# Performance work log

Measured on AMD Instinct MI355X. Metric: run time of the kernel, lower is better.

## Reference

```python
import jax, jax.numpy as jnp
import numpy as np

NODE_W, EDGE_W, HEADS = 512, 32, 8
DOT = NODE_W // HEADS
CLIP_MIN, CLIP_MAX = -5.0, 5.0
B, N = 4, 1024


def setup_inputs() -> dict:
    key = jax.random.key(0)
    ks = jax.random.split(key, 12)
    s = 0.02
    return {
        "nodes": jax.random.normal(ks[0], (B, N, NODE_W), dtype=jnp.float32),
        "edges": jax.random.normal(ks[1], (B, N, N, EDGE_W), dtype=jnp.float32),
        "Wq": jax.random.normal(ks[2], (NODE_W, NODE_W), dtype=jnp.float32) * s,
        "bq": jnp.zeros((NODE_W,), dtype=jnp.float32),
        "Wk": jax.random.normal(ks[3], (NODE_W, NODE_W), dtype=jnp.float32) * s,
        "bk": jnp.zeros((NODE_W,), dtype=jnp.float32),
        "Wv": jax.random.normal(ks[4], (NODE_W, NODE_W), dtype=jnp.float32) * s,
        "bv": jnp.zeros((NODE_W,), dtype=jnp.float32),
        "Wg": jax.random.normal(ks[5], (EDGE_W, HEADS), dtype=jnp.float32) * s,
        "bg": jnp.zeros((HEADS,), dtype=jnp.float32),
        "We": jax.random.normal(ks[6], (EDGE_W, HEADS), dtype=jnp.float32) * s,
        "be": jnp.zeros((HEADS,), dtype=jnp.float32),
    }


def reference(nodes, edges, Wq, bq, Wk, bk, Wv, bv, Wg, bg, We, be):
    b, n, _ = nodes.shape
    # projections, reshaped to [B, N, dot_dim, heads] as in the torch .view
    q = (nodes @ Wq + bq).reshape(b, n, DOT, HEADS)
    k = (nodes @ Wk + bk).reshape(b, n, DOT, HEADS)
    v = (nodes @ Wv + bv).reshape(b, n, DOT, HEADS)
    # raw scores [B, L, M, heads], scaled and clipped
    H = jnp.einsum('bldh,bmdh->blmh', q, k) / (DOT ** 0.5)
    H = jnp.clip(H, CLIP_MIN, CLIP_MAX)
    # edge bias and gate, each [B, N, N, heads]
    e = edges @ We + be
    g = edges @ Wg + bg
    H = H + e
    # softmax over key axis (dim=2), sigmoid gate multiply
    A = jax.nn.sigmoid(g) * jax.nn.softmax(H, axis=2)
    # dropout is identity in eval/deterministic mode
    attn = jnp.einsum('blmh,bmdh->bldh', A, v).reshape(b, n, NODE_W)
    return attn, H
```

## Files before the change

kernel.cpp:

```cpp
#include <hip/hip_runtime.h>
#include <hip/hip_bf16.h>
#include <stdint.h>

typedef float  f32x4  __attribute__((ext_vector_type(4)));
typedef float  f32x2  __attribute__((ext_vector_type(2)));
typedef short  bf16x8 __attribute__((ext_vector_type(8)));
typedef short  bf16x4 __attribute__((ext_vector_type(4)));

#define MFMA16(A,B,C) __builtin_amdgcn_mfma_f32_16x16x32_bf16(A,B,C,0,0,0)

__device__ __forceinline__ short f2bf(float x){
    union { float f; uint32_t u; } v; v.f = x;
    uint32_t r = v.u + 0x7fffu + ((v.u >> 16) & 1u);
    return (short)(r >> 16);
}
__device__ __forceinline__ float bf2f(short x){
    union { uint32_t u; float f; } v; v.u = ((uint32_t)(uint16_t)x) << 16;
    return v.f;
}
__device__ __forceinline__ uint32_t cvt2(float lo, float hi){
    __hip_bfloat162 t = __float22bfloat162_rn(float2{lo, hi});
    union { __hip_bfloat162 b; uint32_t u; } c; c.b = t; return c.u;
}
__device__ __forceinline__ bf16x8 pack8(f32x4 a, f32x4 b){
    union { uint32_t u[4]; bf16x8 s; } c;
    c.u[0] = cvt2(a[0], a[1]); c.u[1] = cvt2(a[2], a[3]);
    c.u[2] = cvt2(b[0], b[1]); c.u[3] = cvt2(b[2], b[3]);
    return c.s;
}

__global__ void k_prep_wt(const float* __restrict__ Wq, const float* __restrict__ Wk,
                          const float* __restrict__ Wv, short* __restrict__ WT){
    int blk = blockIdx.x;
    int w  = blk >> 6;
    int t  = blk & 63;
    int k0 = (t >> 3) << 6;
    int o0 = (t & 7) << 6;
    const float* W = (w == 0) ? Wq : ((w == 1) ? Wk : Wv);
    __shared__ float tile[64][65];
    int tx = threadIdx.x & 63, ty = threadIdx.x >> 6;
    #pragma unroll
    for (int i = 0; i < 64; i += 4)
        tile[ty + i][tx] = W[(size_t)(k0 + ty + i) * 512 + o0 + tx];
    __syncthreads();
    short* out = WT + (size_t)w * 512 * 512;
    #pragma unroll
    for (int i = 0; i < 64; i += 4)
        out[(size_t)(o0 + ty + i) * 512 + k0 + tx] = f2bf(tile[tx][ty + i]);
}

__global__ void k_prep_wcat(const float* __restrict__ We, const float* __restrict__ Wg,
                            const float* __restrict__ be, const float* __restrict__ bg,
                            short* __restrict__ WcatT, float* __restrict__ bcat){
    int t = threadIdx.x;
    int ch = t >> 5, c = t & 31;
    float v = (ch < 8) ? We[c * 8 + ch] : Wg[c * 8 + (ch - 8)];
    WcatT[ch * 32 + c] = f2bf(v);
    if (t < 16) bcat[t] = (t < 8) ? be[t] : bg[t - 8];
}

__global__ void k_prep_nodes(const float* __restrict__ nodes, short* __restrict__ nb){
    size_t i = ((size_t)blockIdx.x * 256 + threadIdx.x) * 8;
    f32x4 a = *(const f32x4*)(nodes + i);
    f32x4 b = *(const f32x4*)(nodes + i + 4);
    *(bf16x8*)(nb + i) = pack8(a, b);
}

__global__ void k_qkv(const short* __restrict__ nodesbf, const short* __restrict__ WT,
                      const float* __restrict__ bq, const float* __restrict__ bk,
                      const float* __restrict__ bv,
                      short* __restrict__ qb, short* __restrict__ kb, short* __restrict__ vTb){
    int bx = blockIdx.x;
    int lt = bx & 255;
    int ob = bx >> 8;
    int wave = threadIdx.x >> 6, lane = threadIdx.x & 63;
    int lr = lane & 15, lg = lane >> 4;
    int row0 = lt << 4;
    int og = ob * 256 + wave * 64;
    int w  = og >> 9;
    int oo = og & 511;
    int dhalf = ob & 1;

    const short* Wp = WT + (size_t)w * 512 * 512;
    f32x4 acc[4] = {};
    const short* arow = nodesbf + (size_t)(row0 + lr) * 512 + lg * 8;
    #pragma unroll
    for (int kk = 0; kk < 16; ++kk){
        bf16x8 af = *(const bf16x8*)(arow + kk * 32);
        #pragma unroll
        for (int s = 0; s < 4; ++s){
            const short* bp = Wp + (size_t)(oo + s * 16 + lr) * 512 + kk * 32 + lg * 8;
            bf16x8 bfv = *(const bf16x8*)bp;
            acc[s] = MFMA16(af, bfv, acc[s]);
        }
    }
    const float* bias = (w == 0) ? bq : ((w == 1) ? bk : bv);
    int b  = row0 >> 10;
    int lbase = row0 & 1023;

    __shared__ short St[4096];
    #pragma unroll
    for (int s = 0; s < 4; ++s){
        int o = oo + s * 16 + lr;
        float bsv = bias[o];
        int h = o & 7, dd = (o >> 3) & 31;
        #pragma unroll
        for (int r = 0; r < 4; ++r){
            short sv = f2bf(acc[s][r] + bsv);
            int l = lg * 4 + r;
            if (w < 2) St[(l << 8) + (h << 5) + dd] = sv;
            else       St[(h << 9) + (dd << 4) + l] = sv;
        }
    }
    __syncthreads();
    int t = threadIdx.x;
    bf16x8 v0 = *(const bf16x8*)&St[t * 16];
    bf16x8 v1 = *(const bf16x8*)&St[t * 16 + 8];
    if (w < 2){
        short* dst = (w == 0) ? qb : kb;
        int l = t >> 4, h = (t >> 1) & 7, dd0 = (t & 1) << 4;
        size_t a = ((size_t)(b * 8 + h) * 1024 + lbase + l) * 64 + dhalf * 32 + dd0;
        *(bf16x8*)(dst + a)     = v0;
        *(bf16x8*)(dst + a + 8) = v1;
    } else {
        int h = t >> 5, dd = t & 31;
        size_t a = ((size_t)(b * 8 + h) * 64 + dhalf * 32 + dd) * 1024 + lbase;
        *(bf16x8*)(vTb + a)     = v0;
        *(bf16x8*)(vTb + a + 8) = v1;
    }
}

__global__ __launch_bounds__(256, 3) void k_hsg(
        const float* __restrict__ edges, const short* __restrict__ qb,
        const short* __restrict__ kb, const short* __restrict__ WcatT,
        const float* __restrict__ bcat,
        float* __restrict__ Hout, short* __restrict__ Pb,
        float* __restrict__ psum){
    int bx = blockIdx.x;
    int j  = bx & 7;  int b = j >> 1;
    int rest = bx >> 3;
    int mt = rest & 15;
    int lt = (rest >> 4) | ((j & 1) << 5);
    int w = threadIdx.x >> 6, lane = threadIdx.x & 63;
    int lr = lane & 15, lg = lane >> 4;
    int l0 = lt << 4;
    int mg = (mt << 6) + (w << 4);
    const size_t bl0 = (size_t)(b * 1024 + l0);

    __shared__ short eg[4][4096];
    char* egw = (char*)&eg[w][0];
    const int swz = (lr & 7) << 4;

    f32x4 ebA[4][2], ebB[4][2];
    #pragma unroll
    for (int i = 0; i < 4; ++i){
        const float* ep = edges + ((bl0 + i) * 1024 + mg + lr) * 32 + lg * 8;
        ebA[i][0] = *(const f32x4*)ep;
        ebA[i][1] = *(const f32x4*)(ep + 4);
    }

    f32x4 S[8] = {};
    #pragma unroll
    for (int h = 0; h < 8; ++h){
        #pragma unroll
        for (int half = 0; half < 2; ++half){
            bf16x8 kf = *(const bf16x8*)(kb + ((size_t)(b * 8 + h) * 1024 + mg + lr) * 64 + half * 32 + lg * 8);
            bf16x8 qf = *(const bf16x8*)(qb + ((size_t)(b * 8 + h) * 1024 + l0 + lr) * 64 + half * 32 + lg * 8);
            S[h] = MFMA16(kf, qf, S[h]);
        }
    }

    bf16x8 wf = *(const bf16x8*)(WcatT + lr * 32 + lg * 8);
    f32x4  bc = *(const f32x4*)(bcat + lg * 4);
    f32x4 zero = {0.f, 0.f, 0.f, 0.f};
    #pragma unroll
    for (int c = 0; c < 4; ++c){
        if (c < 3){
            #pragma unroll
            for (int i = 0; i < 4; ++i){
                const float* ep = edges + ((bl0 + (c + 1) * 4 + i) * 1024 + mg + lr) * 32 + lg * 8;
                if (c & 1){ ebA[i][0] = *(const f32x4*)ep; ebA[i][1] = *(const f32x4*)(ep + 4); }
                else      { ebB[i][0] = *(const f32x4*)ep; ebB[i][1] = *(const f32x4*)(ep + 4); }
            }
        }
        #pragma unroll
        for (int i = 0; i < 4; ++i){
            int l = c * 4 + i;
            f32x4 e0 = (c & 1) ? ebB[i][0] : ebA[i][0];
            f32x4 e1 = (c & 1) ? ebB[i][1] : ebA[i][1];
            f32x4 d = MFMA16(wf, pack8(e0, e1), zero);
            union { uint32_t u[2]; bf16x4 v; } dv;
            dv.u[0] = cvt2(d[0] + bc[0], d[1] + bc[1]);
            dv.u[1] = cvt2(d[2] + bc[2], d[3] + bc[3]);
            int bw = (l * 512 + lr * 32 + lg * 8) ^ ((l & 7) << 4);
            *(bf16x4*)(egw + bw) = dv.v;
        }
    }

    float exu[4][8], pgv[4][8];
    #pragma unroll
    for (int rr = 0; rr < 4; ++rr){
        int base = lr * 512 + (4 * lg + rr) * 32;
        bf16x8 e8 = *(const bf16x8*)(egw + ((base)      ^ swz));
        bf16x8 g8 = *(const bf16x8*)(egw + ((base + 16) ^ swz));
        float Hv[8];
        #pragma unroll
        for (int h = 0; h < 8; ++h){
            float s = S[h][rr] * 0.125f;
            s = fminf(fmaxf(s, -5.f), 5.f);
            float hv = s + bf2f(e8[h]);
            Hv[h] = hv;
            float ex = __expf(hv);
            exu[rr][h] = ex;
            float sg = __builtin_amdgcn_rcpf(1.f + __expf(-bf2f(g8[h])));
            pgv[rr][h] = ex * sg;
        }
        float* hp = Hout + (bl0 + lr) * 8192 + (size_t)(mg + 4 * lg + rr) * 8;
        f32x4 h0 = {Hv[0], Hv[1], Hv[2], Hv[3]};
        f32x4 h1 = {Hv[4], Hv[5], Hv[6], Hv[7]};
        *(f32x4*)hp       = h0;
        *(f32x4*)(hp + 4) = h1;
    }

    size_t ptile = ((size_t)(b * 8) * 64 + lt) * 64 + (mt * 4 + w);
    size_t psbase = (((size_t)(b * 64 + lt) * 16 + mt) * 4 + w) * 128;
    #pragma unroll
    for (int h = 0; h < 8; ++h){
        union { uint32_t u[2]; bf16x4 v; } pv;
        pv.u[0] = cvt2(pgv[0][h], pgv[1][h]);
        pv.u[1] = cvt2(pgv[2][h], pgv[3][h]);
        *(bf16x4*)(Pb + (ptile + (size_t)h * 4096) * 256 + lr * 16 + lg * 4) = pv.v;
        float t = exu[0][h] + exu[1][h] + exu[2][h] + exu[3][h];
        t += __shfl_xor(t, 16);
        t += __shfl_xor(t, 32);
        if (lg == 0) psum[psbase + h * 16 + lr] = t;
    }
}

__global__ void k_pv(const short* __restrict__ Pb, const float* __restrict__ psum,
                     const short* __restrict__ vTb, float* __restrict__ attn){
    int bx = blockIdx.x;
    int j  = bx & 7;  int b = j >> 1;
    int lt = ((j & 1) << 5) | (bx >> 3);
    int h    = threadIdx.x >> 6;
    int lane = threadIdx.x & 63;
    int lr = lane & 15, lg = lane >> 4;
    int l0 = lt << 4;

    const short* Pbase = Pb  + (((size_t)(b * 8 + h) * 64 + lt) * 64) * 256;
    const short* vbase = vTb + (size_t)(b * 8 + h) * 65536;

    f32x4 O[4] = {};
    for (int ks = 0; ks < 32; ++ks){
        bf16x8 pf = *(const bf16x8*)(Pbase + (ks * 2 + (lg >> 1)) * 256 + lr * 16 + (lg & 1) * 8);
        #pragma unroll
        for (int dt = 0; dt < 4; ++dt){
            bf16x8 vf = *(const bf16x8*)(vbase + (size_t)(dt * 16 + lr) * 1024 + ks * 32 + lg * 8);
            O[dt] = MFMA16(vf, pf, O[dt]);
        }
    }

    const float* pp = psum + ((size_t)(b * 64 + lt) * 16) * 512;
    float ds = 0.f;
    #pragma unroll
    for (int c = 0; c < 16; ++c)
        ds += pp[(c * 4 + lg) * 128 + h * 16 + lr];
    ds += __shfl_xor(ds, 16);
    ds += __shfl_xor(ds, 32);
    float inv = __builtin_amdgcn_rcpf(ds);

    __shared__ float Os[16][516];
    #pragma unroll
    for (int dt = 0; dt < 4; ++dt){
        #pragma unroll
        for (int r = 0; r < 4; ++r)
            Os[lr][(dt * 16 + lg * 4 + r) * 8 + h] = O[dt][r] * inv;
    }
    __syncthreads();
    int row = threadIdx.x >> 5;
    int cb  = (threadIdx.x & 31) * 16;
    float* dst = attn + ((size_t)(b * 1024 + l0 + row)) * 512 + cb;
    #pragma unroll
    for (int jj = 0; jj < 16; jj += 4)
        *(f32x4*)(dst + jj) = *(const f32x4*)&Os[row][cb + jj];
}

#define OFF_WT    ((size_t)0x0000000)
#define OFF_WCAT  ((size_t)0x0180000)
#define OFF_BCAT  ((size_t)0x0180400)
#define OFF_NB    ((size_t)0x0200000)
#define OFF_Q     ((size_t)0x0600000)
#define OFF_K     ((size_t)0x0A00000)
#define OFF_VT    ((size_t)0x0E00000)
#define OFF_P     ((size_t)0x1200000)
#define OFF_PS    ((size_t)0x5200000)

extern "C" void kernel_launch(void* const* d_in, const int* in_sizes, int n_in,
                              void* d_out, int out_size, void* d_ws, size_t ws_size,
                              hipStream_t stream) {
    const float* nodes = (const float*)d_in[0];
    const float* edges = (const float*)d_in[1];
    const float* Wq = (const float*)d_in[2];
    const float* bq = (const float*)d_in[3];
    const float* Wk = (const float*)d_in[4];
    const float* bk = (const float*)d_in[5];
    const float* Wv = (const float*)d_in[6];
    const float* bv = (const float*)d_in[7];
    const float* Wg = (const float*)d_in[8];
    const float* bg = (const float*)d_in[9];
    const float* We = (const float*)d_in[10];
    const float* be = (const float*)d_in[11];

    float* out_attn = (float*)d_out;
    float* out_H    = out_attn + (size_t)4 * 1024 * 512;

    char* ws = (char*)d_ws;
    short* WT    = (short*)(ws + OFF_WT);
    short* WcatT = (short*)(ws + OFF_WCAT);
    float* bcat  = (float*)(ws + OFF_BCAT);
    short* nb    = (short*)(ws + OFF_NB);
    short* qb    = (short*)(ws + OFF_Q);
    short* kb    = (short*)(ws + OFF_K);
    short* vTb   = (short*)(ws + OFF_VT);
    short* Pb    = (short*)(ws + OFF_P);
    float* psum  = (float*)(ws + OFF_PS);

    k_prep_wt   <<<192, 256, 0, stream>>>(Wq, Wk, Wv, WT);
    k_prep_wcat <<<1, 512, 0, stream>>>(We, Wg, be, bg, WcatT, bcat);
    k_prep_nodes<<<1024, 256, 0, stream>>>(nodes, nb);
    k_qkv       <<<1536, 256, 0, stream>>>(nb, WT, bq, bk, bv, qb, kb, vTb);
    k_hsg       <<<4096, 256, 0, stream>>>(edges, qb, kb, WcatT, bcat, out_H, Pb, psum);
    k_pv        <<<256, 512, 0, stream>>>(Pb, psum, vTb, out_attn);
}
```

Before: 296.1 us.

## Merge prep kernels, raise hsg occupancy, split PV reduction across waves

Folds the three prep kernels into one launch to save launch overhead. Raises k_hsg launch bounds from 3 to 4 blocks per CU and restructures the softmax epilogue so bf16 packing and denominator sums happen in-loop, which lowers register pressure. Splits k_pv so each block handles 4 heads with two waves per head covering halves of the key range, combined through shared memory. This doubles the block count to improve parallelism in the PV stage. The cost is an extra shared-memory reduction and a possible spill risk in k_hsg.

```diff
diff --git a/kernel.cpp b/kernel.cpp
--- a/kernel.cpp
+++ b/kernel.cpp
@@ -29,41 +29,44 @@
     return c.s;
 }
 
-__global__ void k_prep_wt(const float* __restrict__ Wq, const float* __restrict__ Wk,
-                          const float* __restrict__ Wv, short* __restrict__ WT){
+__global__ void k_prep(const float* __restrict__ Wq, const float* __restrict__ Wk,
+                       const float* __restrict__ Wv, const float* __restrict__ We,
+                       const float* __restrict__ Wg, const float* __restrict__ be,
+                       const float* __restrict__ bg, const float* __restrict__ nodes,
+                       short* __restrict__ WT, short* __restrict__ WcatT,
+                       float* __restrict__ bcat, short* __restrict__ nb){
     int blk = blockIdx.x;
-    int w  = blk >> 6;
-    int t  = blk & 63;
-    int k0 = (t >> 3) << 6;
-    int o0 = (t & 7) << 6;
-    const float* W = (w == 0) ? Wq : ((w == 1) ? Wk : Wv);
-    __shared__ float tile[64][65];
-    int tx = threadIdx.x & 63, ty = threadIdx.x >> 6;
-    #pragma unroll
-    for (int i = 0; i < 64; i += 4)
-        tile[ty + i][tx] = W[(size_t)(k0 + ty + i) * 512 + o0 + tx];
-    __syncthreads();
-    short* out = WT + (size_t)w * 512 * 512;
-    #pragma unroll
-    for (int i = 0; i < 64; i += 4)
-        out[(size_t)(o0 + ty + i) * 512 + k0 + tx] = f2bf(tile[tx][ty + i]);
-}
-
-__global__ void k_prep_wcat(const float* __restrict__ We, const float* __restrict__ Wg,
-                            const float* __restrict__ be, const float* __restrict__ bg,
-                            short* __restrict__ WcatT, float* __restrict__ bcat){
-    int t = threadIdx.x;
-    int ch = t >> 5, c = t & 31;
-    float v = (ch < 8) ? We[c * 8 + ch] : Wg[c * 8 + (ch - 8)];
-    WcatT[ch * 32 + c] = f2bf(v);
-    if (t < 16) bcat[t] = (t < 8) ? be[t] : bg[t - 8];
-}
-
-__global__ void k_prep_nodes(const float* __restrict__ nodes, short* __restrict__ nb){
-    size_t i = ((size_t)blockIdx.x * 256 + threadIdx.x) * 8;
-    f32x4 a = *(const f32x4*)(nodes + i);
-    f32x4 b = *(const f32x4*)(nodes + i + 4);
-    *(bf16x8*)(nb + i) = pack8(a, b);
+    if (blk < 192){
+        int w  = blk >> 6;
+        int t  = blk & 63;
+        int k0 = (t >> 3) << 6;
+        int o0 = (t & 7) << 6;
+        const float* W = (w == 0) ? Wq : ((w == 1) ? Wk : Wv);
+        __shared__ float tile[64][65];
+        int tx = threadIdx.x & 63, ty = threadIdx.x >> 6;
+        #pragma unroll
+        for (int i = 0; i < 64; i += 4)
+            tile[ty + i][tx] = W[(size_t)(k0 + ty + i) * 512 + o0 + tx];
+        __syncthreads();
+        short* out = WT + (size_t)w * 512 * 512;
+        #pragma unroll
+        for (int i = 0; i < 64; i += 4)
+            out[(size_t)(o0 + ty + i) * 512 + k0 + tx] = f2bf(tile[tx][ty + i]);
+    } else if (blk == 192){
+        #pragma unroll
+        for (int i = 0; i < 2; ++i){
+            int t = i * 256 + threadIdx.x;
+            int ch = t >> 5, c = t & 31;
+            float v = (ch < 8) ? We[c * 8 + ch] : Wg[c * 8 + (ch - 8)];
+            WcatT[ch * 32 + c] = f2bf(v);
+        }
+        if (threadIdx.x < 16) bcat[threadIdx.x] = (threadIdx.x < 8) ? be[threadIdx.x] : bg[threadIdx.x - 8];
+    } else {
+        size_t i = ((size_t)(blk - 193) * 256 + threadIdx.x) * 8;
+        f32x4 a = *(const f32x4*)(nodes + i);
+        f32x4 b = *(const f32x4*)(nodes + i + 4);
+        *(bf16x8*)(nb + i) = pack8(a, b);
+    }
 }
 
 __global__ void k_qkv(const short* __restrict__ nodesbf, const short* __restrict__ WT,
@@ -130,7 +133,7 @@
     }
 }
 
-__global__ __launch_bounds__(256, 3) void k_hsg(
+__global__ __launch_bounds__(256, 4) void k_hsg(
         const float* __restrict__ edges, const short* __restrict__ qb,
         const short* __restrict__ kb, const short* __restrict__ WcatT,
         const float* __restrict__ bcat,
@@ -197,29 +200,37 @@
         }
     }
 
-    float exu[4][8], pgv[4][8];
-    #pragma unroll
-    for (int rr = 0; rr < 4; ++rr){
-        int base = lr * 512 + (4 * lg + rr) * 32;
-        bf16x8 e8 = *(const bf16x8*)(egw + ((base)      ^ swz));
-        bf16x8 g8 = *(const bf16x8*)(egw + ((base + 16) ^ swz));
-        float Hv[8];
-        #pragma unroll
-        for (int h = 0; h < 8; ++h){
-            float s = S[h][rr] * 0.125f;
-            s = fminf(fmaxf(s, -5.f), 5.f);
-            float hv = s + bf2f(e8[h]);
-            Hv[h] = hv;
-            float ex = __expf(hv);
-            exu[rr][h] = ex;
-            float sg = __builtin_amdgcn_rcpf(1.f + __expf(-bf2f(g8[h])));
-            pgv[rr][h] = ex * sg;
-        }
-        float* hp = Hout + (bl0 + lr) * 8192 + (size_t)(mg + 4 * lg + rr) * 8;
-        f32x4 h0 = {Hv[0], Hv[1], Hv[2], Hv[3]};
-        f32x4 h1 = {Hv[4], Hv[5], Hv[6], Hv[7]};
-        *(f32x4*)hp       = h0;
-        *(f32x4*)(hp + 4) = h1;
+    float dsum[8] = {0.f,0.f,0.f,0.f,0.f,0.f,0.f,0.f};
+    uint32_t pu[2][8];
+    #pragma unroll
+    for (int pr = 0; pr < 2; ++pr){
+        float pgE[8];
+        #pragma unroll
+        for (int rr2 = 0; rr2 < 2; ++rr2){
+            int rr = pr * 2 + rr2;
+            int base = lr * 512 + (4 * lg + rr) * 32;
+            bf16x8 e8 = *(const bf16x8*)(egw + ((base)      ^ swz));
+            bf16x8 g8 = *(const bf16x8*)(egw + ((base + 16) ^ swz));
+            float Hv[8];
+            #pragma unroll
+            for (int h = 0; h < 8; ++h){
+                float s = S[h][rr] * 0.125f;
+                s = fminf(fmaxf(s, -5.f), 5.f);
+                float hv = s + bf2f(e8[h]);
+                Hv[h] = hv;
+                float ex = __expf(hv);
+                dsum[h] += ex;
+                float sg = __builtin_amdgcn_rcpf(1.f + __expf(-bf2f(g8[h])));
+                float pg = ex * sg;
+                if (rr2 == 0) pgE[h] = pg;
+                else          pu[pr][h] = cvt2(pgE[h], pg);
+            }
+            float* hp = Hout + (bl0 + lr) * 8192 + (size_t)(mg + 4 * lg + rr) * 8;
+            f32x4 h0 = {Hv[0], Hv[1], Hv[2], Hv[3]};
+            f32x4 h1 = {Hv[4], Hv[5], Hv[6], Hv[7]};
+            *(f32x4*)hp       = h0;
+            *(f32x4*)(hp + 4) = h1;
+        }
     }
 
     size_t ptile = ((size_t)(b * 8) * 64 + lt) * 64 + (mt * 4 + w);
@@ -227,10 +238,9 @@
     #pragma unroll
     for (int h = 0; h < 8; ++h){
         union { uint32_t u[2]; bf16x4 v; } pv;
-        pv.u[0] = cvt2(pgv[0][h], pgv[1][h]);
-        pv.u[1] = cvt2(pgv[2][h], pgv[3][h]);
+        pv.u[0] = pu[0][h]; pv.u[1] = pu[1][h];
         *(bf16x4*)(Pb + (ptile + (size_t)h * 4096) * 256 + lr * 16 + lg * 4) = pv.v;
-        float t = exu[0][h] + exu[1][h] + exu[2][h] + exu[3][h];
+        float t = dsum[h];
         t += __shfl_xor(t, 16);
         t += __shfl_xor(t, 32);
         if (lg == 0) psum[psbase + h * 16 + lr] = t;
@@ -241,17 +251,21 @@
                      const short* __restrict__ vTb, float* __restrict__ attn){
     int bx = blockIdx.x;
     int j  = bx & 7;  int b = j >> 1;
-    int lt = ((j & 1) << 5) | (bx >> 3);
-    int h    = threadIdx.x >> 6;
+    int rest = bx >> 3;
+    int hg = rest >> 5;
+    int lt = ((j & 1) << 5) | (rest & 31);
+    int w    = threadIdx.x >> 6;
     int lane = threadIdx.x & 63;
     int lr = lane & 15, lg = lane >> 4;
     int l0 = lt << 4;
-
-    const short* Pbase = Pb  + (((size_t)(b * 8 + h) * 64 + lt) * 64) * 256;
-    const short* vbase = vTb + (size_t)(b * 8 + h) * 65536;
+    int head = hg * 4 + (w >> 1);
+    int half = w & 1;
+
+    const short* Pbase = Pb  + (((size_t)(b * 8 + head) * 64 + lt) * 64) * 256;
+    const short* vbase = vTb + (size_t)(b * 8 + head) * 65536;
 
     f32x4 O[4] = {};
-    for (int ks = 0; ks < 32; ++ks){
+    for (int ks = half * 16; ks < half * 16 + 16; ++ks){
         bf16x8 pf = *(const bf16x8*)(Pbase + (ks * 2 + (lg >> 1)) * 256 + lr * 16 + (lg & 1) * 8);
         #pragma unroll
         for (int dt = 0; dt < 4; ++dt){
@@ -264,25 +278,37 @@
     float ds = 0.f;
     #pragma unroll
     for (int c = 0; c < 16; ++c)
-        ds += pp[(c * 4 + lg) * 128 + h * 16 + lr];
+        ds += pp[(c * 4 + lg) * 128 + head * 16 + lr];
     ds += __shfl_xor(ds, 16);
     ds += __shfl_xor(ds, 32);
     float inv = __builtin_amdgcn_rcpf(ds);
 
-    __shared__ float Os[16][516];
-    #pragma unroll
-    for (int dt = 0; dt < 4; ++dt){
-        #pragma unroll
-        for (int r = 0; r < 4; ++r)
-            Os[lr][(dt * 16 + lg * 4 + r) * 8 + h] = O[dt][r] * inv;
+    __shared__ float Opart[4][16][64];
+    __shared__ float Os[16][260];
+    if (half == 1){
+        #pragma unroll
+        for (int dt = 0; dt < 4; ++dt)
+            #pragma unroll
+            for (int r = 0; r < 4; ++r)
+                Opart[w >> 1][lr][dt * 16 + lg * 4 + r] = O[dt][r];
+    }
+    __syncthreads();
+    if (half == 0){
+        #pragma unroll
+        for (int dt = 0; dt < 4; ++dt)
+            #pragma unroll
+            for (int r = 0; r < 4; ++r){
+                int d = dt * 16 + lg * 4 + r;
+                float o = O[dt][r] + Opart[w >> 1][lr][d];
+                Os[lr][d * 4 + (w >> 1)] = o * inv;
+            }
     }
     __syncthreads();
     int row = threadIdx.x >> 5;
-    int cb  = (threadIdx.x & 31) * 16;
-    float* dst = attn + ((size_t)(b * 1024 + l0 + row)) * 512 + cb;
-    #pragma unroll
-    for (int jj = 0; jj < 16; jj += 4)
-        *(f32x4*)(dst + jj) = *(const f32x4*)&Os[row][cb + jj];
+    int c0  = (threadIdx.x & 31) * 8;
+    float* dst = attn + ((size_t)(b * 1024 + l0 + row)) * 512 + (threadIdx.x & 31) * 16 + hg * 4;
+    *(f32x4*)dst       = *(const f32x4*)&Os[row][c0];
+    *(f32x4*)(dst + 8) = *(const f32x4*)&Os[row][c0 + 4];
 }
 
 #define OFF_WT    ((size_t)0x0000000)
@@ -325,10 +351,9 @@
     short* Pb    = (short*)(ws + OFF_P);
     float* psum  = (float*)(ws + OFF_PS);
 
-    k_prep_wt   <<<192, 256, 0, stream>>>(Wq, Wk, Wv, WT);
-    k_prep_wcat <<<1, 512, 0, stream>>>(We, Wg, be, bg, WcatT, bcat);
-    k_prep_nodes<<<1024, 256, 0, stream>>>(nodes, nb);
-    k_qkv       <<<1536, 256, 0, stream>>>(nb, WT, bq, bk, bv, qb, kb, vTb);
-    k_hsg       <<<4096, 256, 0, stream>>>(edges, qb, kb, WcatT, bcat, out_H, Pb, psum);
-    k_pv        <<<256, 512, 0, stream>>>(Pb, psum, vTb, out_attn);
-}
+    k_prep <<<1217, 256, 0, stream>>>(Wq, Wk, Wv, We, Wg, be, bg, nodes,
+                                      WT, WcatT, bcat, nb);
+    k_qkv  <<<1536, 256, 0, stream>>>(nb, WT, bq, bk, bv, qb, kb, vTb);
+    k_hsg  <<<4096, 256, 0, stream>>>(edges, qb, kb, WcatT, bcat, out_H, Pb, psum);
+    k_pv   <<<512, 512, 0, stream>>>(Pb, psum, vTb, out_attn);
+}
```

Measured after the change: 291.9 us. No clear change (-1.4%).
